# Performance work log

Measured on AMD Instinct MI355X. Metric: run time of the kernel, lower is better.

The kernel has to match this reference:

```python
import jax, jax.numpy as jnp
import numpy as np

NUM_EMBEDDINGS = 512
EMBEDDING_DIM = 64


def setup_inputs() -> dict:
    key = jax.random.key(0)
    k1, k2 = jax.random.split(key)
    z_e = jax.random.normal(k1, (32, EMBEDDING_DIM, 64, 64), dtype=jnp.float32)
    lim = 1.0 / NUM_EMBEDDINGS
    codebook = jax.random.uniform(k2, (NUM_EMBEDDINGS, EMBEDDING_DIM),
                                  dtype=jnp.float32, minval=-lim, maxval=lim)
    return {"z_e": z_e, "codebook": codebook}


def reference(z_e, codebook):
    B, C, H, W = z_e.shape
    # [B,C,H,W] -> [N, C] with N = B*H*W (channels-last flatten)
    z_flat = jnp.transpose(z_e, (0, 2, 3, 1)).reshape(-1, C)
    # squared L2 distance via ||a||^2 + ||b||^2 - 2 a.b (same math, no NxKxC tensor)
    d = (jnp.sum(z_flat * z_flat, axis=1, keepdims=True)          # [N,1]
         + jnp.sum(codebook * codebook, axis=1)[None, :]           # [1,K]
         - 2.0 * jnp.einsum('nc,kc->nk', z_flat, codebook))        # [N,K]
    encoding_indices = jnp.argmin(d, axis=1)                       # [N] int
    z_q = codebook[encoding_indices].reshape(B, H, W, C)
    z_q = jnp.transpose(z_q, (0, 3, 1, 2))                         # [B,C,H,W]
    return z_q, encoding_indices
```

## Files before the change

kernel.cpp:

```cpp
#include <hip/hip_runtime.h>
#include <stdint.h>


#pragma clang fp contract(off)

#define KCODES 512
#define CDIM 64
#define HW 4096
#define ZQ_ELEMS 8388608

typedef float f2 __attribute__((ext_vector_type(2)));

static __device__ __forceinline__ f2 pk_fma_s(f2 a, uint64_t b, f2 c) {
    f2 d;
    asm("v_pk_fma_f32 %0, %1, %2, %3" : "=v"(d) : "v"(a), "s"(b), "v"(c));
    return d;
}
static __device__ __forceinline__ f2 pk_add(f2 a, f2 b) {
    f2 d;
    asm("v_pk_add_f32 %0, %1, %2" : "=v"(d) : "v"(a), "v"(b));
    return d;
}

static __device__ __forceinline__ float cnorm_row(const float* __restrict__ row) {
    float r[8];
    #pragma unroll
    for (int j = 0; j < 8; ++j) r[j] = row[j] * row[j];
    #pragma unroll
    for (int i = 8; i < 64; i += 8) {
        #pragma unroll
        for (int j = 0; j < 8; ++j) r[j] = r[j] + row[i + j] * row[i + j];
    }
    return ((r[0] + r[1]) + (r[2] + r[3])) + ((r[4] + r[5]) + (r[6] + r[7]));
}

__global__ void cnorm_kernel(const float* __restrict__ cb,
                             float* __restrict__ cnorm_out) {
    int k = (int)blockIdx.x * 256 + (int)threadIdx.x;
    if (k < KCODES) cnorm_out[k] = cnorm_row(cb + (size_t)k * CDIM);
}

__global__ __launch_bounds__(256)
__attribute__((amdgpu_waves_per_eu(2)))
void vq_kernel(
    const float* __restrict__ z_e,
    const float* __restrict__ cb,
    const float* __restrict__ cnorm_g,
    float* __restrict__ out)
{
    __shared__ float cnorm[KCODES];
    __shared__ float dcand[4 * 64];
    __shared__ int   kcand[4 * 64];

    if (cnorm_g) {
        #pragma unroll
        for (int k = (int)threadIdx.x; k < KCODES; k += 256)
            cnorm[k] = cnorm_g[k];
    } else {
        for (int k = (int)threadIdx.x; k < KCODES; k += 256)
            cnorm[k] = cnorm_row(cb + (size_t)k * CDIM);
    }

    const int lane = (int)threadIdx.x & 63;
    const int g = __builtin_amdgcn_readfirstlane((int)threadIdx.x >> 6);
    const int n0 = (int)blockIdx.x * 64;
    const int b = n0 / HW;
    const int hw0 = n0 % HW;
    const float* zp = z_e + (size_t)b * CDIM * HW + hw0 + lane;

    f2 zz2[CDIM / 2];
    #pragma unroll
    for (int m = 0; m < CDIM / 2; ++m) {
        f2 t;
        t.x = zp[(size_t)(2 * m) * HW];
        t.y = zp[(size_t)(2 * m + 1) * HW];
        zz2[m] = t;
    }

    float sz;
    {
        f2 pr[4];
        #pragma unroll
        for (int t = 0; t < 4; ++t) pr[t] = zz2[t] * zz2[t];
        #pragma unroll
        for (int i = 8; i < 64; i += 8) {
            #pragma unroll
            for (int t = 0; t < 4; ++t) {
                f2 zt = zz2[(i + 2 * t) / 2];
                pr[t] = pr[t] + zt * zt;
            }
        }
        float s01 = pr[0].x + pr[0].y;
        float s23 = pr[1].x + pr[1].y;
        float s45 = pr[2].x + pr[2].y;
        float s67 = pr[3].x + pr[3].y;
        sz = (s01 + s23) + (s45 + s67);
    }

    __syncthreads();

    f2 zero; zero.x = 0.f; zero.y = 0.f;

    float best = 3.4e38f;
    int bk = 0;
    const int k0 = g * 128;

    for (int i = 0; i < 128; ++i) {
        const int k = k0 + i;
        const float* ck = cb + k * CDIM;
        const uint64_t* cq = (const uint64_t*)(const void*)ck;

        f2 pv[8];
        #pragma unroll
        for (int j = 0; j < 8; ++j) {
            pv[j] = pk_fma_s(zz2[j], cq[j],
                      pk_fma_s(zz2[8 + j], cq[8 + j],
                        pk_fma_s(zz2[16 + j], cq[16 + j],
                          pk_fma_s(zz2[24 + j], cq[24 + j], zero))));
        }
        f2 pe0 = pk_add(pv[0], pv[4]), pe1 = pk_add(pv[1], pv[5]);
        f2 pe2 = pk_add(pv[2], pv[6]), pe3 = pk_add(pv[3], pv[7]);
        f2 pf0 = pk_add(pe0, pe2), pf1 = pk_add(pe1, pe3);
        f2 pt = pk_add(pf0, pf1);
        float dot = pt.x + pt.y;

        float A = sz + cnorm[k];
        float d = fmaf(dot, -2.f, A);

        if (d < best) { best = d; bk = k; }
    }

    dcand[g * 64 + lane] = best;
    kcand[g * 64 + lane] = bk;
    __syncthreads();

    float bd = dcand[lane];
    int bi = kcand[lane];
    #pragma unroll
    for (int gg = 1; gg < 4; ++gg) {
        float d2 = dcand[gg * 64 + lane];
        int   k2 = kcand[gg * 64 + lane];
        if (d2 < bd) { bd = d2; bi = k2; }
    }

    if (g == 0) out[ZQ_ELEMS + n0 + lane] = (float)bi;

    const float* row = cb + (size_t)bi * CDIM;
    float* op = out + (size_t)b * CDIM * HW + hw0 + lane;
    #pragma unroll
    for (int c = 0; c < 16; ++c) {
        const int ch = g * 16 + c;
        op[(size_t)ch * HW] = row[ch];
    }
}

extern "C" void kernel_launch(void* const* d_in, const int* in_sizes, int n_in,
                              void* d_out, int out_size, void* d_ws, size_t ws_size,
                              hipStream_t stream) {
    const float* z_e = (const float*)d_in[0];
    const float* cb  = (const float*)d_in[1];
    float* out = (float*)d_out;

    float* cnorm_ws = nullptr;
    if (ws_size >= KCODES * sizeof(float)) {
        cnorm_ws = (float*)d_ws;
        cnorm_kernel<<<dim3(2), dim3(256), 0, stream>>>(cb, cnorm_ws);
    }
    vq_kernel<<<dim3(2048), dim3(256), 0, stream>>>(z_e, cb, cnorm_ws, out);
}
```

Measured before the change: 193.6 us.

## Use single-wave blocks scanning all codes with scalar FMAs instead of packed split

Each 64-thread block now has one wave scan all 512 codes per pixel. Before, four waves each covered 128 codes and merged their candidates through shared memory. The packed v_pk_fma inline asm is replaced by plain scalar fmaf, and the gather of z_q rows uses float4 loads. This removes the cross-wave reduction and a barrier, but it quarters the thread count per block, quadruples the serial loop length per wave, and may lose packed-math throughput.

After: 255.5 us. +32.0%, slower.

```diff
diff --git a/kernel.cpp b/kernel.cpp
--- a/kernel.cpp
+++ b/kernel.cpp
@@ -8,19 +8,6 @@
 #define CDIM 64
 #define HW 4096
 #define ZQ_ELEMS 8388608
-
-typedef float f2 __attribute__((ext_vector_type(2)));
-
-static __device__ __forceinline__ f2 pk_fma_s(f2 a, uint64_t b, f2 c) {
-    f2 d;
-    asm("v_pk_fma_f32 %0, %1, %2, %3" : "=v"(d) : "v"(a), "s"(b), "v"(c));
-    return d;
-}
-static __device__ __forceinline__ f2 pk_add(f2 a, f2 b) {
-    f2 d;
-    asm("v_pk_add_f32 %0, %1, %2" : "=v"(d) : "v"(a), "v"(b));
-    return d;
-}
 
 static __device__ __forceinline__ float cnorm_row(const float* __restrict__ row) {
     float r[8];
@@ -40,8 +27,7 @@
     if (k < KCODES) cnorm_out[k] = cnorm_row(cb + (size_t)k * CDIM);
 }
 
-__global__ __launch_bounds__(256)
-__attribute__((amdgpu_waves_per_eu(2)))
+__global__ __launch_bounds__(64)
 void vq_kernel(
     const float* __restrict__ z_e,
     const float* __restrict__ cb,
@@ -49,80 +35,66 @@
     float* __restrict__ out)
 {
     __shared__ float cnorm[KCODES];
-    __shared__ float dcand[4 * 64];
-    __shared__ int   kcand[4 * 64];
+
+    const int lane = (int)threadIdx.x;
 
     if (cnorm_g) {
         #pragma unroll
-        for (int k = (int)threadIdx.x; k < KCODES; k += 256)
+        for (int k = lane; k < KCODES; k += 64)
             cnorm[k] = cnorm_g[k];
     } else {
-        for (int k = (int)threadIdx.x; k < KCODES; k += 256)
+        for (int k = lane; k < KCODES; k += 64)
             cnorm[k] = cnorm_row(cb + (size_t)k * CDIM);
     }
 
-    const int lane = (int)threadIdx.x & 63;
-    const int g = __builtin_amdgcn_readfirstlane((int)threadIdx.x >> 6);
     const int n0 = (int)blockIdx.x * 64;
     const int b = n0 / HW;
     const int hw0 = n0 % HW;
     const float* zp = z_e + (size_t)b * CDIM * HW + hw0 + lane;
 
-    f2 zz2[CDIM / 2];
+    float zz[CDIM];
     #pragma unroll
-    for (int m = 0; m < CDIM / 2; ++m) {
-        f2 t;
-        t.x = zp[(size_t)(2 * m) * HW];
-        t.y = zp[(size_t)(2 * m + 1) * HW];
-        zz2[m] = t;
-    }
+    for (int m = 0; m < CDIM; ++m)
+        zz[m] = zp[(size_t)m * HW];
 
     float sz;
     {
-        f2 pr[4];
+        float r[8];
         #pragma unroll
-        for (int t = 0; t < 4; ++t) pr[t] = zz2[t] * zz2[t];
+        for (int j = 0; j < 8; ++j) r[j] = zz[j] * zz[j];
         #pragma unroll
         for (int i = 8; i < 64; i += 8) {
             #pragma unroll
-            for (int t = 0; t < 4; ++t) {
-                f2 zt = zz2[(i + 2 * t) / 2];
-                pr[t] = pr[t] + zt * zt;
-            }
+            for (int j = 0; j < 8; ++j) r[j] = r[j] + zz[i + j] * zz[i + j];
         }
-        float s01 = pr[0].x + pr[0].y;
-        float s23 = pr[1].x + pr[1].y;
-        float s45 = pr[2].x + pr[2].y;
-        float s67 = pr[3].x + pr[3].y;
-        sz = (s01 + s23) + (s45 + s67);
+        sz = ((r[0] + r[1]) + (r[2] + r[3])) + ((r[4] + r[5]) + (r[6] + r[7]));
     }
 
     __syncthreads();
 
-    f2 zero; zero.x = 0.f; zero.y = 0.f;
-
     float best = 3.4e38f;
     int bk = 0;
-    const int k0 = g * 128;
 
-    for (int i = 0; i < 128; ++i) {
-        const int k = k0 + i;
-        const float* ck = cb + k * CDIM;
-        const uint64_t* cq = (const uint64_t*)(const void*)ck;
+    for (int k = 0; k < KCODES; ++k) {
+        const float* ck = cb + (size_t)k * CDIM;
 
-        f2 pv[8];
+        float v[16];
         #pragma unroll
-        for (int j = 0; j < 8; ++j) {
-            pv[j] = pk_fma_s(zz2[j], cq[j],
-                      pk_fma_s(zz2[8 + j], cq[8 + j],
-                        pk_fma_s(zz2[16 + j], cq[16 + j],
-                          pk_fma_s(zz2[24 + j], cq[24 + j], zero))));
-        }
-        f2 pe0 = pk_add(pv[0], pv[4]), pe1 = pk_add(pv[1], pv[5]);
-        f2 pe2 = pk_add(pv[2], pv[6]), pe3 = pk_add(pv[3], pv[7]);
-        f2 pf0 = pk_add(pe0, pe2), pf1 = pk_add(pe1, pe3);
-        f2 pt = pk_add(pf0, pf1);
-        float dot = pt.x + pt.y;
+        for (int l = 0; l < 16; ++l)
+            v[l] = fmaf(zz[l], ck[l],
+                     fmaf(zz[16 + l], ck[16 + l],
+                       fmaf(zz[32 + l], ck[32 + l],
+                         fmaf(zz[48 + l], ck[48 + l], 0.f))));
+
+        float e[8];
+        #pragma unroll
+        for (int l = 0; l < 8; ++l) e[l] = v[l] + v[8 + l];
+        float f[4];
+        #pragma unroll
+        for (int l = 0; l < 4; ++l) f[l] = e[l] + e[4 + l];
+        float g0 = f[0] + f[2];
+        float g1 = f[1] + f[3];
+        float dot = g0 + g1;
 
         float A = sz + cnorm[k];
         float d = fmaf(dot, -2.f, A);
@@ -130,27 +102,17 @@
         if (d < best) { best = d; bk = k; }
     }
 
-    dcand[g * 64 + lane] = best;
-    kcand[g * 64 + lane] = bk;
-    __syncthreads();
+    out[ZQ_ELEMS + n0 + lane] = (float)bk;
 
-    float bd = dcand[lane];
-    int bi = kcand[lane];
-    #pragma unroll
-    for (int gg = 1; gg < 4; ++gg) {
-        float d2 = dcand[gg * 64 + lane];
-        int   k2 = kcand[gg * 64 + lane];
-        if (d2 < bd) { bd = d2; bi = k2; }
-    }
-
-    if (g == 0) out[ZQ_ELEMS + n0 + lane] = (float)bi;
-
-    const float* row = cb + (size_t)bi * CDIM;
+    const float* row = cb + (size_t)bk * CDIM;
     float* op = out + (size_t)b * CDIM * HW + hw0 + lane;
     #pragma unroll
-    for (int c = 0; c < 16; ++c) {
-        const int ch = g * 16 + c;
-        op[(size_t)ch * HW] = row[ch];
+    for (int c4 = 0; c4 < 16; ++c4) {
+        float4 t = ((const float4*)row)[c4];
+        op[(size_t)(4 * c4 + 0) * HW] = t.x;
+        op[(size_t)(4 * c4 + 1) * HW] = t.y;
+        op[(size_t)(4 * c4 + 2) * HW] = t.z;
+        op[(size_t)(4 * c4 + 3) * HW] = t.w;
     }
 }
 
@@ -166,5 +128,5 @@
         cnorm_ws = (float*)d_ws;
         cnorm_kernel<<<dim3(2), dim3(256), 0, stream>>>(cb, cnorm_ws);
     }
-    vq_kernel<<<dim3(2048), dim3(256), 0, stream>>>(z_e, cb, cnorm_ws, out);
+    vq_kernel<<<dim3(2048), dim3(64), 0, stream>>>(z_e, cb, cnorm_ws, out);
 }
```
